# Kernel optimization log

Hardware: AMD Instinct MI355X
Metric: run time of the kernel (lower is better)

Reference implementation:

```python
import jax, jax.numpy as jnp
import numpy as np
import math

IN_C, N_EMBD, HEADS = 256, 512, 8

def setup_inputs() -> dict:
    key = jax.random.key(0)
    ks = jax.random.split(key, 5)
    B, T = 64, 500
    x = jax.random.normal(ks[0], (B, T, IN_C), dtype=jnp.float32)
    # torch Linear: y = x @ W.T + b; store W as [out, in]
    w_attn = jax.random.normal(ks[1], (3 * N_EMBD, IN_C), dtype=jnp.float32) * (1.0 / math.sqrt(IN_C))
    b_attn = jax.random.normal(ks[2], (3 * N_EMBD,), dtype=jnp.float32) * 0.02
    w_proj = jax.random.normal(ks[3], (N_EMBD, N_EMBD), dtype=jnp.float32) * (1.0 / math.sqrt(N_EMBD))
    b_proj = jax.random.normal(ks[4], (N_EMBD,), dtype=jnp.float32) * 0.02
    return {"x": x, "w_attn": w_attn, "b_attn": b_attn, "w_proj": w_proj, "b_proj": b_proj}

def reference(x, w_attn, b_attn, w_proj, b_proj):
    B, T, C = x.shape
    H, D = HEADS, N_EMBD // HEADS
    qkv = jnp.einsum('btc,ec->bte', x, w_attn) + b_attn  # [B,T,3*n_embd]
    q, k, v = jnp.split(qkv, 3, axis=-1)
    # [B,T,n_embd] -> [B,H,T,D]
    q = q.reshape(B, T, H, D).transpose(0, 2, 1, 3)
    k = k.reshape(B, T, H, D).transpose(0, 2, 1, 3)
    v = v.reshape(B, T, H, D).transpose(0, 2, 1, 3)
    att = jnp.einsum('bhtd,bhsd->bhts', q, k) * (1.0 / math.sqrt(D))
    # bias buffer is all-ones: masked_fill(bias==0, -inf) is a no-op
    att = jax.nn.softmax(att, axis=-1)
    y = jnp.einsum('bhts,bhsd->bhtd', att, v)  # [B,H,T,D]
    y = y.transpose(0, 2, 1, 3).reshape(B, T, N_EMBD)
    return jnp.einsum('bte,fe->btf', y, w_proj) + b_proj
```

## Files before the change

### kernel.cpp

```cpp
#include <hip/hip_runtime.h>

typedef _Float16 f16;
typedef _Float16 f16x8 __attribute__((ext_vector_type(8)));
typedef _Float16 f16x2 __attribute__((ext_vector_type(2)));
typedef float    f32x4 __attribute__((ext_vector_type(4)));
typedef float    f32x16 __attribute__((ext_vector_type(16)));
typedef unsigned int u32;

typedef const __attribute__((address_space(1))) void GVOID;
typedef __attribute__((address_space(3))) void LVOID;

static __device__ __forceinline__ f32x4 mfma16(f16x8 a, f16x8 b, f32x4 c) {
  return __builtin_amdgcn_mfma_f32_16x16x32_f16(a, b, c, 0, 0, 0);
}
static __device__ __forceinline__ f32x16 mfma32(f16x8 a, f16x8 b, f32x16 c) {
  return __builtin_amdgcn_mfma_f32_32x32x16_f16(a, b, c, 0, 0, 0);
}
static __device__ __forceinline__ void gl_lds16(const f16* g, f16* l) {
  __builtin_amdgcn_global_load_lds((GVOID*)g, (LVOID*)l, 16, 0, 0);
}
static __device__ __forceinline__ u32 pk(float a, float b) {
  union { f16x2 h; u32 w; } u;
  u.h[0] = (f16)a; u.h[1] = (f16)b;
  return u.w;
}
static __device__ __forceinline__ f16x8 mkfrag(float a0, float a1, float a2, float a3,
                                               float a4, float a5, float a6, float a7) {
  u32 c01 = pk(a0, a1), c23 = pk(a2, a3), c45 = pk(a4, a5), c67 = pk(a6, a7);
  asm("v_permlane32_swap_b32 %0, %1" : "+v"(c01), "+v"(c45));
  asm("v_permlane32_swap_b32 %0, %1" : "+v"(c23), "+v"(c67));
  union { f16x8 h; u32 w[4]; } u;
  u.w[0] = c01; u.w[1] = c23; u.w[2] = c45; u.w[3] = c67;
  return u.h;
}

__global__ __launch_bounds__(256)
void cvt_kernel(const float* __restrict__ s, f16* __restrict__ d, int n) {
  int i = (blockIdx.x * 256 + threadIdx.x) * 8;
  if (i >= n) return;
  float4 v0 = *(const float4*)(s + i);
  float4 v1 = *(const float4*)(s + i + 4);
  f16x8 h;
  h[0] = (f16)v0.x; h[1] = (f16)v0.y; h[2] = (f16)v0.z; h[3] = (f16)v0.w;
  h[4] = (f16)v1.x; h[5] = (f16)v1.y; h[6] = (f16)v1.z; h[7] = (f16)v1.w;
  *(f16x8*)(d + i) = h;
}

template<int EPI, int KD, int NDIM>
__global__ __launch_bounds__(256)
void gemm16(const f16* __restrict__ A, const f16* __restrict__ B,
            const float* __restrict__ bias, f16* __restrict__ outH,
            float* __restrict__ outF) {
  constexpr int NB = NDIM / 128;
  const int cpx = gridDim.x >> 3;
  const int id = blockIdx.x;
  const int g = (id & 7) * cpx + (id >> 3);
  const int mb = g / NB, nb = g - mb * NB;
  const int m0 = mb * 128, n0 = nb * 128;

  __shared__ __align__(16) f16 As[128 * 64];
  __shared__ __align__(16) f16 Bs[128 * 64];
  const int tid = threadIdx.x, lane = tid & 63, wid = tid >> 6;
  const int wm = (wid >> 1) * 64, wn = (wid & 1) * 64;
  const int fr = lane & 15, fg = lane >> 4;

  f32x4 acc[4][4] = {};

  for (int k0 = 0; k0 < KD; k0 += 64) {
    __syncthreads();
#pragma unroll
    for (int i = 0; i < 4; ++i) {
      int ca = i * 256 + tid;
      int row = ca >> 3, col = (ca & 7) * 8;
      gl_lds16(A + (size_t)(m0 + row) * KD + k0 + col, &As[ca * 8]);
      gl_lds16(B + (size_t)(n0 + row) * KD + k0 + col, &Bs[ca * 8]);
    }
    __syncthreads();
#pragma unroll
    for (int kk = 0; kk < 2; ++kk) {
      f16x8 af[4], bf[4];
#pragma unroll
      for (int t = 0; t < 4; ++t) {
        af[t] = *(const f16x8*)&As[(wm + t * 16 + fr) * 64 + kk * 32 + fg * 8];
        bf[t] = *(const f16x8*)&Bs[(wn + t * 16 + fr) * 64 + kk * 32 + fg * 8];
      }
#pragma unroll
      for (int mt = 0; mt < 4; ++mt)
#pragma unroll
        for (int nt = 0; nt < 4; ++nt)
          acc[mt][nt] = mfma16(af[mt], bf[nt], acc[mt][nt]);
    }
  }

  float bv[4];
#pragma unroll
  for (int nt = 0; nt < 4; ++nt) bv[nt] = bias[n0 + wn + nt * 16 + fr];
#pragma unroll
  for (int mt = 0; mt < 4; ++mt) {
    int mg = m0 + wm + mt * 16 + fg * 4;
#pragma unroll
    for (int r = 0; r < 4; ++r)
#pragma unroll
      for (int nt = 0; nt < 4; ++nt) {
        int ng = n0 + wn + nt * 16 + fr;
        float v = acc[mt][nt][r] + bv[nt];
        if (EPI == 0) outH[(size_t)(mg + r) * NDIM + ng] = (f16)v;
        else          outF[(size_t)(mg + r) * NDIM + ng] = v;
      }
  }
}

__global__ __launch_bounds__(256)
void attn_kern(const f16* __restrict__ qkv, f16* __restrict__ Yg) {
  __shared__ __align__(16) f16 Kl[2][64 * 64];
  __shared__ __align__(16) f16 VT[2][64 * 64];
  const int id = blockIdx.x;
  const int g = (id & 7) * 256 + (id >> 3);
  const int bh = g >> 2, qt = g & 3;
  const int b = bh >> 3, h = bh & 7;
  const int tid = threadIdx.x, lane = tid & 63, w = tid >> 6;
  const int l31 = lane & 31, hi = lane >> 5, e7 = l31 & 7;

  const f16* base  = qkv + (size_t)b * 500 * 1536 + h * 64;
  const f16* Kbase = base + 512;
  const f16* Vbase = base + 1024;

  const int q = qt * 128 + w * 32 + l31;
  const int qc = q < 500 ? q : 499;
  f16x8 qf[4];
  const f16* qp = base + (size_t)qc * 1536 + hi * 8;
#pragma unroll
  for (int ds = 0; ds < 4; ++ds) qf[ds] = *(const f16x8*)(qp + 16 * ds);
  const f16 qs = (f16)(0.125f * 1.44269504f);
#pragma unroll
  for (int ds = 0; ds < 4; ++ds)
#pragma unroll
    for (int j = 0; j < 8; ++j) qf[ds][j] *= qs;

  f32x16 O0 = {}, O1 = {};
  float m = -1e30f, l = 0.f;

  const int kvl = tid & 63, d0 = (tid >> 6) * 16;

  {
#pragma unroll
    for (int i = 0; i < 2; ++i) {
      int c = tid + 256 * i, row = c >> 3;
      int col = 8 * ((c & 7) ^ (row & 7));
      gl_lds16(Kbase + (size_t)row * 1536 + col, &Kl[0][c * 8]);
    }
    const f16* vp = Vbase + (size_t)kvl * 1536 + d0;
    f16x8 va = *(const f16x8*)vp, vb = *(const f16x8*)(vp + 8);
    __syncthreads();
#pragma unroll
    for (int j = 0; j < 16; ++j) {
      int d = d0 + j;
      VT[0][64 * d + (kvl ^ ((d & 7) << 3))] = j < 8 ? va[j] : vb[j - 8];
    }
    __syncthreads();
  }

#pragma unroll 2
  for (int kt = 0; kt < 8; ++kt) {
    const int cur = kt & 1;
    f16x8 va, vb;
    if (kt < 7) {
      const int kvn = (kt + 1) * 64;
#pragma unroll
      for (int i = 0; i < 2; ++i) {
        int c = tid + 256 * i, row = c >> 3;
        int kv = kvn + row; kv = kv < 500 ? kv : 499;
        int col = 8 * ((c & 7) ^ (row & 7));
        gl_lds16(Kbase + (size_t)kv * 1536 + col, &Kl[cur ^ 1][c * 8]);
      }
      int kv = kvn + kvl; kv = kv < 500 ? kv : 499;
      const f16* vp = Vbase + (size_t)kv * 1536 + d0;
      va = *(const f16x8*)vp; vb = *(const f16x8*)(vp + 8);
    }

    f32x16 s0 = {}, s1 = {};
#pragma unroll
    for (int ds = 0; ds < 4; ++ds) {
      f16x8 k0 = *(const f16x8*)&Kl[cur][l31 * 64 + 8 * ((hi + 2 * ds) ^ e7)];
      f16x8 k1 = *(const f16x8*)&Kl[cur][(32 + l31) * 64 + 8 * ((hi + 2 * ds) ^ e7)];
      s0 = mfma32(k0, qf[ds], s0);
      s1 = mfma32(k1, qf[ds], s1);
    }

    float p0[16], p1[16];
#pragma unroll
    for (int r = 0; r < 16; ++r) { p0[r] = s0[r]; p1[r] = s1[r]; }
    if (kt == 7) {
#pragma unroll
      for (int r = 0; r < 16; ++r) {
        int kvL = (r & 3) + 8 * (r >> 2) + 4 * hi;
        if (480 + kvL >= 500) p1[r] = -1e30f;
      }
    }

    float pm = p0[0];
#pragma unroll
    for (int r = 1; r < 16; ++r) pm = fmaxf(pm, p0[r]);
#pragma unroll
    for (int r = 0; r < 16; ++r) pm = fmaxf(pm, p1[r]);
    pm = fmaxf(pm, __shfl_xor(pm, 32));

    if (__any(pm - m > 8.f)) {
      float mn = fmaxf(m, pm);
      float fac = __builtin_amdgcn_exp2f(m - mn);
      m = mn; l *= fac;
#pragma unroll
      for (int r = 0; r < 16; ++r) {
        int rowv = (r & 3) + 8 * (r >> 2) + 4 * hi;
        float fr_ = __shfl(fac, rowv);
        O0[r] *= fr_; O1[r] *= fr_;
      }
    }

    float ps = 0.f;
#pragma unroll
    for (int r = 0; r < 16; ++r) { float t = __builtin_amdgcn_exp2f(p0[r] - m); p0[r] = t; ps += t; }
#pragma unroll
    for (int r = 0; r < 16; ++r) { float t = __builtin_amdgcn_exp2f(p1[r] - m); p1[r] = t; ps += t; }
    ps += __shfl_xor(ps, 32);
    l += ps;

    f16x8 pf0 = mkfrag(p0[0], p0[1], p0[2], p0[3], p0[4], p0[5], p0[6], p0[7]);
    f16x8 pf1 = mkfrag(p0[8], p0[9], p0[10], p0[11], p0[12], p0[13], p0[14], p0[15]);
    f16x8 pf2 = mkfrag(p1[0], p1[1], p1[2], p1[3], p1[4], p1[5], p1[6], p1[7]);
    f16x8 pf3 = mkfrag(p1[8], p1[9], p1[10], p1[11], p1[12], p1[13], p1[14], p1[15]);

#pragma unroll
    for (int ks = 0; ks < 4; ++ks) {
      f16x8 pf = ks == 0 ? pf0 : ks == 1 ? pf1 : ks == 2 ? pf2 : pf3;
      int sw = (16 * ks + 8 * hi) ^ (e7 << 3);
      f16x8 v0 = *(const f16x8*)&VT[cur][l31 * 64 + sw];
      f16x8 v1 = *(const f16x8*)&VT[cur][(32 + l31) * 64 + sw];
      O0 = mfma32(pf, v0, O0);
      O1 = mfma32(pf, v1, O1);
    }

    __syncthreads();
    if (kt < 7) {
#pragma unroll
      for (int j = 0; j < 16; ++j) {
        int d = d0 + j;
        VT[cur ^ 1][64 * d + (kvl ^ ((d & 7) << 3))] = j < 8 ? va[j] : vb[j - 8];
      }
      __syncthreads();
    }
  }

  float linv = 1.f / l;
#pragma unroll
  for (int r = 0; r < 16; ++r) {
    int rowv = (r & 3) + 8 * (r >> 2) + 4 * hi;
    float li = __shfl(linv, rowv);
    int t = qt * 128 + w * 32 + rowv;
    if (t < 500) {
      size_t rowb = (size_t)(b * 500 + t) * 512 + h * 64;
      Yg[rowb + l31]      = (f16)(O0[r] * li);
      Yg[rowb + 32 + l31] = (f16)(O1[r] * li);
    }
  }
}

extern "C" void kernel_launch(void* const* d_in, const int* in_sizes, int n_in,
                              void* d_out, int out_size, void* d_ws, size_t ws_size,
                              hipStream_t stream) {
  const float* x      = (const float*)d_in[0];
  const float* w_attn = (const float*)d_in[1];
  const float* b_attn = (const float*)d_in[2];
  const float* w_proj = (const float*)d_in[3];
  const float* b_proj = (const float*)d_in[4];
  float* out = (float*)d_out;

  char* wsp = (char*)d_ws;
  f16* Yg   = (f16*)wsp;
  f16* x_h  = (f16*)wsp;
  f16* qkv  = (f16*)(wsp + 32768000);
  f16* wa_h = (f16*)(wsp + 32768000 + 98304000);
  f16* wp_h = (f16*)(wsp + 32768000 + 98304000 + 786432);
  if (ws_size < 132382720) return;

  dim3 blk(256);
  cvt_kernel<<<4000, blk, 0, stream>>>(x, x_h, 8192000);
  cvt_kernel<<<192,  blk, 0, stream>>>(w_attn, wa_h, 393216);
  cvt_kernel<<<128,  blk, 0, stream>>>(w_proj, wp_h, 262144);

  gemm16<0, 256, 1536><<<3000, blk, 0, stream>>>(x_h, wa_h, b_attn, qkv, nullptr);
  attn_kern<<<2048, blk, 0, stream>>>(qkv, Yg);
  gemm16<1, 512, 512><<<1000, blk, 0, stream>>>(Yg, wp_h, b_proj, nullptr, out);
}
```

Before: 154.9 us.

## Swizzle GEMM LDS, compute softmax row sums via MFMA, restructure V transpose

The GEMM kernel now stores A/B tiles in LDS with an XOR swizzle so fragment reads avoid bank conflicts. In attention, the softmax denominator is accumulated by an extra MFMA against a ones vector instead of VALU sums and cross-lane shuffles. V is transposed into LDS with packed half2 stores covering two kv rows per lane, and out-of-range kv rows are zeroed. The loop uses one barrier per tile instead of two and raises wave priority around MFMA blocks. The trade-off is extra MFMA work per tile and a write into the next V buffer before the barrier, which depends on the double buffer being safe to reuse.

```diff
diff --git a/kernel.cpp b/kernel.cpp
--- a/kernel.cpp
+++ b/kernel.cpp
@@ -63,6 +63,7 @@
   const int tid = threadIdx.x, lane = tid & 63, wid = tid >> 6;
   const int wm = (wid >> 1) * 64, wn = (wid & 1) * 64;
   const int fr = lane & 15, fg = lane >> 4;
+  const int e7 = fr & 7;
 
   f32x4 acc[4][4] = {};
 
@@ -70,19 +71,21 @@
     __syncthreads();
 #pragma unroll
     for (int i = 0; i < 4; ++i) {
-      int ca = i * 256 + tid;
-      int row = ca >> 3, col = (ca & 7) * 8;
-      gl_lds16(A + (size_t)(m0 + row) * KD + k0 + col, &As[ca * 8]);
-      gl_lds16(B + (size_t)(n0 + row) * KD + k0 + col, &Bs[ca * 8]);
+      int c = i * 256 + tid;
+      int row = c >> 3;
+      int col = 8 * ((c & 7) ^ (row & 7));
+      gl_lds16(A + (size_t)(m0 + row) * KD + k0 + col, &As[c * 8]);
+      gl_lds16(B + (size_t)(n0 + row) * KD + k0 + col, &Bs[c * 8]);
     }
     __syncthreads();
 #pragma unroll
     for (int kk = 0; kk < 2; ++kk) {
+      const int sa = 8 * ((4 * kk + fg) ^ e7);
       f16x8 af[4], bf[4];
 #pragma unroll
       for (int t = 0; t < 4; ++t) {
-        af[t] = *(const f16x8*)&As[(wm + t * 16 + fr) * 64 + kk * 32 + fg * 8];
-        bf[t] = *(const f16x8*)&Bs[(wn + t * 16 + fr) * 64 + kk * 32 + fg * 8];
+        af[t] = *(const f16x8*)&As[(wm + t * 16 + fr) * 64 + sa];
+        bf[t] = *(const f16x8*)&Bs[(wn + t * 16 + fr) * 64 + sa];
       }
 #pragma unroll
       for (int mt = 0; mt < 4; ++mt)
@@ -137,10 +140,16 @@
 #pragma unroll
     for (int j = 0; j < 8; ++j) qf[ds][j] *= qs;
 
-  f32x16 O0 = {}, O1 = {};
-  float m = -1e30f, l = 0.f;
-
-  const int kvl = tid & 63, d0 = (tid >> 6) * 16;
+  f16x8 ONE;
+#pragma unroll
+  for (int j = 0; j < 8; ++j) ONE[j] = (f16)1.f;
+
+  f32x16 O0 = {}, O1 = {}, La = {};
+  float m = -1e30f;
+
+  const int kvp = (lane & 31) * 2, dh = (lane >> 5) * 8, d0 = w * 16;
+  f16x8 va, vb;
+  const f16x8 VZ = {};
 
   {
 #pragma unroll
@@ -149,21 +158,19 @@
       int col = 8 * ((c & 7) ^ (row & 7));
       gl_lds16(Kbase + (size_t)row * 1536 + col, &Kl[0][c * 8]);
     }
-    const f16* vp = Vbase + (size_t)kvl * 1536 + d0;
-    f16x8 va = *(const f16x8*)vp, vb = *(const f16x8*)(vp + 8);
-    __syncthreads();
-#pragma unroll
-    for (int j = 0; j < 16; ++j) {
-      int d = d0 + j;
-      VT[0][64 * d + (kvl ^ ((d & 7) << 3))] = j < 8 ? va[j] : vb[j - 8];
+    const f16* vp = Vbase + (size_t)kvp * 1536 + d0 + dh;
+    va = *(const f16x8*)vp; vb = *(const f16x8*)(vp + 1536);
+#pragma unroll
+    for (int j = 0; j < 8; ++j) {
+      f16x2 p2; p2[0] = va[j]; p2[1] = vb[j];
+      *(f16x2*)&VT[0][(d0 + dh + j) * 64 + (kvp ^ (j << 3))] = p2;
     }
     __syncthreads();
   }
 
 #pragma unroll 2
   for (int kt = 0; kt < 8; ++kt) {
-    const int cur = kt & 1;
-    f16x8 va, vb;
+    const int cur = kt & 1, nxt = cur ^ 1;
     if (kt < 7) {
       const int kvn = (kt + 1) * 64;
 #pragma unroll
@@ -171,14 +178,19 @@
         int c = tid + 256 * i, row = c >> 3;
         int kv = kvn + row; kv = kv < 500 ? kv : 499;
         int col = 8 * ((c & 7) ^ (row & 7));
-        gl_lds16(Kbase + (size_t)kv * 1536 + col, &Kl[cur ^ 1][c * 8]);
-      }
-      int kv = kvn + kvl; kv = kv < 500 ? kv : 499;
-      const f16* vp = Vbase + (size_t)kv * 1536 + d0;
-      va = *(const f16x8*)vp; vb = *(const f16x8*)(vp + 8);
+        gl_lds16(Kbase + (size_t)kv * 1536 + col, &Kl[nxt][c * 8]);
+      }
+      int kv = kvn + kvp;
+      int kc0 = kv < 500 ? kv : 499, kc1 = kv + 1 < 500 ? kv + 1 : 499;
+      const f16* vp0 = Vbase + (size_t)kc0 * 1536 + d0 + dh;
+      const f16* vp1 = Vbase + (size_t)kc1 * 1536 + d0 + dh;
+      va = *(const f16x8*)vp0; vb = *(const f16x8*)(vp1);
+      if (kv >= 500) va = VZ;
+      if (kv + 1 >= 500) vb = VZ;
     }
 
     f32x16 s0 = {}, s1 = {};
+    __builtin_amdgcn_s_setprio(1);
 #pragma unroll
     for (int ds = 0; ds < 4; ++ds) {
       f16x8 k0 = *(const f16x8*)&Kl[cur][l31 * 64 + 8 * ((hi + 2 * ds) ^ e7)];
@@ -186,50 +198,44 @@
       s0 = mfma32(k0, qf[ds], s0);
       s1 = mfma32(k1, qf[ds], s1);
     }
-
-    float p0[16], p1[16];
-#pragma unroll
-    for (int r = 0; r < 16; ++r) { p0[r] = s0[r]; p1[r] = s1[r]; }
+    __builtin_amdgcn_s_setprio(0);
+
     if (kt == 7) {
 #pragma unroll
       for (int r = 0; r < 16; ++r) {
         int kvL = (r & 3) + 8 * (r >> 2) + 4 * hi;
-        if (480 + kvL >= 500) p1[r] = -1e30f;
-      }
-    }
-
-    float pm = p0[0];
-#pragma unroll
-    for (int r = 1; r < 16; ++r) pm = fmaxf(pm, p0[r]);
-#pragma unroll
-    for (int r = 0; r < 16; ++r) pm = fmaxf(pm, p1[r]);
+        if (480 + kvL >= 500) s1[r] = -1e30f;
+      }
+    }
+
+    float pm = fmaxf(s0[0], s1[0]);
+#pragma unroll
+    for (int r = 1; r < 16; ++r) pm = fmaxf(pm, fmaxf(s0[r], s1[r]));
     pm = fmaxf(pm, __shfl_xor(pm, 32));
 
     if (__any(pm - m > 8.f)) {
       float mn = fmaxf(m, pm);
       float fac = __builtin_amdgcn_exp2f(m - mn);
-      m = mn; l *= fac;
+      m = mn;
 #pragma unroll
       for (int r = 0; r < 16; ++r) {
         int rowv = (r & 3) + 8 * (r >> 2) + 4 * hi;
         float fr_ = __shfl(fac, rowv);
-        O0[r] *= fr_; O1[r] *= fr_;
-      }
-    }
-
-    float ps = 0.f;
-#pragma unroll
-    for (int r = 0; r < 16; ++r) { float t = __builtin_amdgcn_exp2f(p0[r] - m); p0[r] = t; ps += t; }
-#pragma unroll
-    for (int r = 0; r < 16; ++r) { float t = __builtin_amdgcn_exp2f(p1[r] - m); p1[r] = t; ps += t; }
-    ps += __shfl_xor(ps, 32);
-    l += ps;
-
-    f16x8 pf0 = mkfrag(p0[0], p0[1], p0[2], p0[3], p0[4], p0[5], p0[6], p0[7]);
-    f16x8 pf1 = mkfrag(p0[8], p0[9], p0[10], p0[11], p0[12], p0[13], p0[14], p0[15]);
-    f16x8 pf2 = mkfrag(p1[0], p1[1], p1[2], p1[3], p1[4], p1[5], p1[6], p1[7]);
-    f16x8 pf3 = mkfrag(p1[8], p1[9], p1[10], p1[11], p1[12], p1[13], p1[14], p1[15]);
-
+        O0[r] *= fr_; O1[r] *= fr_; La[r] *= fr_;
+      }
+    }
+
+#pragma unroll
+    for (int r = 0; r < 16; ++r) s0[r] = __builtin_amdgcn_exp2f(s0[r] - m);
+#pragma unroll
+    for (int r = 0; r < 16; ++r) s1[r] = __builtin_amdgcn_exp2f(s1[r] - m);
+
+    f16x8 pf0 = mkfrag(s0[0], s0[1], s0[2], s0[3], s0[4], s0[5], s0[6], s0[7]);
+    f16x8 pf1 = mkfrag(s0[8], s0[9], s0[10], s0[11], s0[12], s0[13], s0[14], s0[15]);
+    f16x8 pf2 = mkfrag(s1[0], s1[1], s1[2], s1[3], s1[4], s1[5], s1[6], s1[7]);
+    f16x8 pf3 = mkfrag(s1[8], s1[9], s1[10], s1[11], s1[12], s1[13], s1[14], s1[15]);
+
+    __builtin_amdgcn_s_setprio(1);
 #pragma unroll
     for (int ks = 0; ks < 4; ++ks) {
       f16x8 pf = ks == 0 ? pf0 : ks == 1 ? pf1 : ks == 2 ? pf2 : pf3;
@@ -238,26 +244,26 @@
       f16x8 v1 = *(const f16x8*)&VT[cur][(32 + l31) * 64 + sw];
       O0 = mfma32(pf, v0, O0);
       O1 = mfma32(pf, v1, O1);
-    }
-
+      La = mfma32(pf, ONE, La);
+    }
+    __builtin_amdgcn_s_setprio(0);
+
+    if (kt < 7) {
+#pragma unroll
+      for (int j = 0; j < 8; ++j) {
+        f16x2 p2; p2[0] = va[j]; p2[1] = vb[j];
+        *(f16x2*)&VT[nxt][(d0 + dh + j) * 64 + (kvp ^ (j << 3))] = p2;
+      }
+    }
     __syncthreads();
-    if (kt < 7) {
-#pragma unroll
-      for (int j = 0; j < 16; ++j) {
-        int d = d0 + j;
-        VT[cur ^ 1][64 * d + (kvl ^ ((d & 7) << 3))] = j < 8 ? va[j] : vb[j - 8];
-      }
-      __syncthreads();
-    }
-  }
-
-  float linv = 1.f / l;
+  }
+
 #pragma unroll
   for (int r = 0; r < 16; ++r) {
     int rowv = (r & 3) + 8 * (r >> 2) + 4 * hi;
-    float li = __shfl(linv, rowv);
     int t = qt * 128 + w * 32 + rowv;
     if (t < 500) {
+      float li = __builtin_amdgcn_rcpf(La[r]);
       size_t rowb = (size_t)(b * 500 + t) * 512 + h * 64;
       Yg[rowb + l31]      = (f16)(O0[r] * li);
       Yg[rowb + 32 + l31] = (f16)(O1[r] * li);
```

New measurement: 200.0 us. +29.2%, slower.
